# Kernel optimization log

Measured on AMD Instinct MI355X. Metric: run time of the kernel, lower is better.

Reference implementation:

```python
import jax, jax.numpy as jnp
import numpy as np

NUM_HEADS = 8  # matches init_kwargs


def setup_inputs() -> dict:
    key = jax.random.key(0)
    k_x, k_q, k_k, k_v, k_o = jax.random.split(key, 5)
    C = 512
    scale = 1.0 / np.sqrt(C).astype(np.float32)
    return {
        "x": jax.random.normal(k_x, (4, C, 1024), dtype=jnp.float32),
        "Wq": jax.random.normal(k_q, (C, C), dtype=jnp.float32) * scale,
        "Wk": jax.random.normal(k_k, (C, C), dtype=jnp.float32) * scale,
        "Wv": jax.random.normal(k_v, (C, C), dtype=jnp.float32) * scale,
        "Wo": jax.random.normal(k_o, (C, C), dtype=jnp.float32) * scale,
    }


def reference(x, Wq, Wk, Wv, Wo):
    # x: (b, C, n). Conv1d with kernel size 1 and no bias == channel matmul.
    b, C, n = x.shape
    H = NUM_HEADS
    d = C // H  # truncated_planes

    # 1x1 conv projections: (o, c) x (b, c, n) -> (b, o, n)
    q = jnp.einsum("oc,bcn->bon", Wq, x).reshape(b * H, d, n)
    k = jnp.einsum("oc,bcn->bon", Wk, x).reshape(b * H, d, n)
    v = jnp.einsum("oc,bcn->bon", Wv, x).reshape(b * H, d, n)

    # SelfAttention, embedded-gaussian mode (non-local block style, no 1/sqrt(d) scale):
    # scores[bh, i, j] = q[:, i] . k[:, j]; softmax over j; y = attn @ v
    scores = jnp.einsum("hdi,hdj->hij", q, k)       # (b*H, n, n)
    attn = jax.nn.softmax(scores, axis=-1)
    y = jnp.einsum("hij,hdj->hdi", attn, v)          # (b*H, d, n)

    y = y.reshape(b, C, n)
    out = jnp.einsum("oc,bcn->bon", Wo, y)           # final 1x1 conv
    return out
```

## Files before the change

### kernel.cpp

```cpp
#include <hip/hip_runtime.h>

typedef __attribute__((ext_vector_type(8))) short short8;
typedef __attribute__((ext_vector_type(8))) _Float16 half8;
typedef __attribute__((ext_vector_type(4))) float floatx4;
typedef __attribute__((ext_vector_type(4))) float floatv4;
typedef __attribute__((ext_vector_type(4))) short short4v;
typedef __attribute__((ext_vector_type(4))) unsigned short ushort4v;
typedef unsigned short u16;

#define MFMA_BF16(a,b,c) __builtin_amdgcn_mfma_f32_16x16x32_bf16((a),(b),(c),0,0,0)
#define MFMA_F16(a,b,c)  __builtin_amdgcn_mfma_f32_16x16x32_f16((a),(b),(c),0,0,0)

__device__ __forceinline__ u16 f2bf(float f) {
    union { float f; unsigned u; } v; v.f = f;
    unsigned r = (v.u + 0x7fffu + ((v.u >> 16) & 1u)) >> 16;
    return (u16)r;
}
__device__ __forceinline__ float bf2f(u16 h) {
    union { unsigned u; float f; } v; v.u = ((unsigned)h) << 16;
    return v.f;
}
__device__ __forceinline__ u16 f2h(float f) {
    union { _Float16 h; u16 u; } v; v.h = (_Float16)f;
    return v.u;
}

__device__ __forceinline__ void gll16(const u16* g, u16* l) {
    __builtin_amdgcn_global_load_lds(
        (const __attribute__((address_space(1))) void*)g,
        (__attribute__((address_space(3))) void*)l, 16, 0, 0);
}

__global__ __launch_bounds__(256) void prep_kernel(
    const void* __restrict__ x,
    const void* __restrict__ Wq, const void* __restrict__ Wk,
    const void* __restrict__ Wv, const void* __restrict__ Wo,
    u16* __restrict__ xT,
    u16* __restrict__ Wqh, u16* __restrict__ Wkh,
    u16* __restrict__ Wvh, u16* __restrict__ Woh,
    int* __restrict__ flag)
{
    __shared__ float tile[64][65];
    __shared__ int sflag;
    const int tid = threadIdx.x;

    if (tid < 64) {
        u16 u = ((const u16*)x)[2 * tid];
        int e = (u >> 7) & 0xFF;
        unsigned long long m = __ballot(e >= 96 && e <= 140);
        if (tid == 0) sflag = (__popcll(m) >= 40) ? 0 : 1;
    }
    __syncthreads();
    const int isf32 = sflag;
    const int bid = blockIdx.x;
    if (bid == 0 && tid == 0) *flag = isf32;

    if (bid < 512) {
        const int b = bid >> 7, rem = bid & 127;
        const int c0 = (rem >> 4) * 64, n0 = (rem & 15) * 64;
        const int cr = tid >> 4;
        const int n4 = (tid & 15) * 4;
        const size_t base = (size_t)b * 512 * 1024;
        #pragma unroll
        for (int i = 0; i < 4; ++i) {
            int c = i * 16 + cr;
            size_t idx = base + (size_t)(c0 + c) * 1024 + n0 + n4;
            float v0, v1, v2, v3;
            if (isf32) {
                floatv4 v = *(const floatv4*)((const float*)x + idx);
                v0 = v[0]; v1 = v[1]; v2 = v[2]; v3 = v[3];
            } else {
                ushort4v u = *(const ushort4v*)((const u16*)x + idx);
                v0 = bf2f(u[0]); v1 = bf2f(u[1]); v2 = bf2f(u[2]); v3 = bf2f(u[3]);
            }
            tile[c][n4 + 0] = v0; tile[c][n4 + 1] = v1;
            tile[c][n4 + 2] = v2; tile[c][n4 + 3] = v3;
        }
        __syncthreads();
        const int nr = tid >> 4;
        const int c4 = (tid & 15) * 4;
        #pragma unroll
        for (int i = 0; i < 4; ++i) {
            int n = i * 16 + nr;
            short4v o;
            o[0] = (short)f2h(tile[c4 + 0][n]);
            o[1] = (short)f2h(tile[c4 + 1][n]);
            o[2] = (short)f2h(tile[c4 + 2][n]);
            o[3] = (short)f2h(tile[c4 + 3][n]);
            *(short4v*)(xT + ((size_t)b * 1024 + n0 + n) * 512 + c0 + c4) = o;
        }
    } else {
        const int b2 = bid - 512;
        #pragma unroll
        for (int m = 0; m < 4; ++m) {
            const void* src = (m == 0) ? Wq : (m == 1) ? Wk : (m == 2) ? Wv : Wo;
            u16* dst = (m == 0) ? Wqh : (m == 1) ? Wkh : (m == 2) ? Wvh : Woh;
            #pragma unroll
            for (int j = 0; j < 4; ++j) {
                int i = b2 * 4096 + j * 1024 + tid * 4;
                short4v o;
                if (isf32) {
                    floatv4 v = *(const floatv4*)((const float*)src + i);
                    o[0] = (short)f2h(v[0]); o[1] = (short)f2h(v[1]);
                    o[2] = (short)f2h(v[2]); o[3] = (short)f2h(v[3]);
                } else {
                    ushort4v u = *(const ushort4v*)((const u16*)src + i);
                    o[0] = (short)f2h(bf2f(u[0])); o[1] = (short)f2h(bf2f(u[1]));
                    o[2] = (short)f2h(bf2f(u[2])); o[3] = (short)f2h(bf2f(u[3]));
                }
                *(short4v*)(dst + i) = o;
            }
        }
    }
}

__device__ __forceinline__ void stage_1t(
    const u16* __restrict__ A, const u16* __restrict__ B,
    u16* L, int k0, int wave, int srow, int koff)
{
    #pragma unroll
    for (int i = 0; i < 3; ++i) {
        int idx = wave + i * 4;
        const u16* s;
        if (idx < 4) s = A + (idx * 16 + srow) * 512 + k0 + koff;
        else         s = B + ((idx - 4) * 16 + srow) * 512 + k0 + koff;
        gll16(s, L + idx * 512);
    }
}

__device__ __forceinline__ void gemm_1t(
    const u16* __restrict__ A, const u16* __restrict__ B,
    u16* lds, floatx4 acc[2][4], int lane, int wave)
{
    const int quad = lane >> 4, l16 = lane & 15;
    const int msub = (wave & 1) * 32, nsub = (wave >> 1) * 64;
    const int srow = lane >> 2;
    const int koff = (((lane & 3) - (srow >> 1)) & 3) * 8;
    const int pA = ((quad + (l16 >> 1)) & 3) * 8;

    stage_1t(A, B, lds, 0, wave, srow, koff);
    for (int k0 = 0; k0 < 512; k0 += 32) {
        __syncthreads();
        u16* L = lds + ((k0 >> 5) & 1) * 6144;
        if (k0 + 32 < 512)
            stage_1t(A, B, lds + (((k0 >> 5) + 1) & 1) * 6144,
                     k0 + 32, wave, srow, koff);

        half8 ah[2], bh[4];
        #pragma unroll
        for (int mt = 0; mt < 2; ++mt)
            ah[mt] = *(const half8*)(L + (msub + mt * 16 + l16) * 32 + pA);
        #pragma unroll
        for (int nt = 0; nt < 4; ++nt)
            bh[nt] = *(const half8*)(L + 2048 + (nsub + nt * 16 + l16) * 32 + pA);
        #pragma unroll
        for (int mt = 0; mt < 2; ++mt)
            #pragma unroll
            for (int nt = 0; nt < 4; ++nt)
                acc[mt][nt] = MFMA_F16(ah[mt], bh[nt], acc[mt][nt]);
    }
}

__global__ __launch_bounds__(256) void proj_kernel(
    const u16* __restrict__ xT,
    const u16* __restrict__ Wqh, const u16* __restrict__ Wkh,
    const u16* __restrict__ Wvh,
    u16* __restrict__ qT, u16* __restrict__ kT,
    u16* __restrict__ vbuf)
{
    __shared__ u16 lds[12288];
    const int lane = threadIdx.x & 63;
    const int wave = threadIdx.x >> 6;
    const int quad = lane >> 4, l16 = lane & 15;
    const int idx = blockIdx.x;
    const int msub = (wave & 1) * 32, nsub = (wave >> 1) * 64;

    floatx4 acc[2][4];
    #pragma unroll
    for (int i = 0; i < 2; ++i)
        #pragma unroll
        for (int j = 0; j < 4; ++j) acc[i][j] = (floatx4){0.f, 0.f, 0.f, 0.f};

    if (idx < 512) {
        const int w = idx >> 8;
        const int rem = idx & 255;
        const int m0 = (rem >> 2) * 64;
        const int oblk = (rem & 3) * 128;
        gemm_1t(xT + (size_t)m0 * 512, ((w == 0) ? Wqh : Wkh) + oblk * 512,
                lds, acc, lane, wave);

        u16* dst = (w == 0) ? qT : kT;
        #pragma unroll
        for (int mt = 0; mt < 2; ++mt)
            #pragma unroll
            for (int r = 0; r < 4; ++r) {
                int row = m0 + msub + mt * 16 + quad * 4 + r;
                int b = row >> 10, n = row & 1023;
                #pragma unroll
                for (int nt = 0; nt < 4; ++nt) {
                    int o = oblk + nsub + nt * 16 + l16;
                    int head = b * 8 + (o >> 6);
                    int dd = o & 63;
                    dst[(head * 1024 + n) * 64 + dd] = f2h(acc[mt][nt][r]);
                }
            }
    } else {
        const int rem = idx - 512;
        const int m0 = (rem >> 5) * 64;
        const int nblk = (rem & 31) * 128;
        gemm_1t(Wvh + m0 * 512, xT + (size_t)nblk * 512, lds, acc, lane, wave);

        #pragma unroll
        for (int mt = 0; mt < 2; ++mt)
            #pragma unroll
            for (int r = 0; r < 4; ++r) {
                int o = m0 + msub + mt * 16 + quad * 4 + r;
                #pragma unroll
                for (int nt = 0; nt < 4; ++nt) {
                    int col = nblk + nsub + nt * 16 + l16;
                    int b = col >> 10, n = col & 1023;
                    vbuf[b * 524288 + o * 1024 + n] = f2bf(acc[mt][nt][r]);
                }
            }
    }
}

__global__ __launch_bounds__(512) void attn_kernel(
    const u16* __restrict__ qT, const u16* __restrict__ kT,
    const u16* __restrict__ vbuf,
    u16* __restrict__ yT)
{
    __shared__ u16 lds[16384];
    const int lane = threadIdx.x & 63;
    const int wave = threadIdx.x >> 6;
    const int quad = lane >> 4, l16 = lane & 15;
    const int head = blockIdx.x;
    const int i0 = blockIdx.y * 128 + wave * 16;
    const int b = head >> 3, h = head & 7;
    const u16* qp = qT + head * 65536;
    const u16* kp = kT + head * 65536;
    const u16* vb = vbuf + b * 524288 + h * 65536;
    const int srow = lane >> 2;
    const int koff = (((lane & 3) - (srow >> 1)) & 3) * 8;
    const int pA = ((quad + (l16 >> 1)) & 3) * 8;

    const int qoff = (i0 + l16) * 64 + quad * 8;
    half8 aq0 = *(const half8*)(qp + qoff);
    half8 aq1 = *(const half8*)(qp + qoff + 32);

    float lsum = 0.f;
    floatx4 oacc[4];
    #pragma unroll
    for (int dt = 0; dt < 4; ++dt) oacc[dt] = (floatx4){0.f, 0.f, 0.f, 0.f};

    const float L2E = 1.44269504f;
    const float C2  = 69.2493619f;

    auto stage_kv = [&](int j0, u16* L) {
        #pragma unroll
        for (int i = 0; i < 2; ++i) {
            int c = wave + i * 8;
            const u16* s;
            if (c < 8) {
                int kc = c >> 2, r0 = (c & 3) * 16;
                s = kp + (j0 + r0 + srow) * 64 + kc * 32 + koff;
            } else {
                int c8 = c - 8, js = c8 >> 2, r0 = (c8 & 3) * 16;
                s = vb + (r0 + srow) * 1024 + j0 + js * 32 + koff;
            }
            gll16(s, L + c * 512);
        }
    };

    stage_kv(0, lds);

    const int srcA = (quad & 1) * 32 + l16;
    const int srcB = srcA + 16;
    const bool hi = (quad >> 1) != 0;

    for (int j0 = 0; j0 < 1024; j0 += 64) {
        __syncthreads();
        u16* L = lds + ((j0 >> 6) & 1) * 8192;
        if (j0 + 64 < 1024)
            stage_kv(j0 + 64, lds + (((j0 >> 6) + 1) & 1) * 8192);

        unsigned pk[4][2];
        #pragma unroll
        for (int jt = 0; jt < 4; ++jt) {
            int off = jt * 512 + l16 * 32 + pA;
            half8 kh0 = *(const half8*)(L + off);
            half8 kh1 = *(const half8*)(L + 2048 + off);
            floatx4 s = {0.f, 0.f, 0.f, 0.f};
            s = MFMA_F16(kh0, aq0, s);
            s = MFMA_F16(kh1, aq1, s);
            float p0 = __builtin_amdgcn_exp2f(s[0] * L2E - C2);
            float p1 = __builtin_amdgcn_exp2f(s[1] * L2E - C2);
            float p2 = __builtin_amdgcn_exp2f(s[2] * L2E - C2);
            float p3 = __builtin_amdgcn_exp2f(s[3] * L2E - C2);
            lsum += (p0 + p1) + (p2 + p3);
            pk[jt][0] = (unsigned)f2bf(p0) | ((unsigned)f2bf(p1) << 16);
            pk[jt][1] = (unsigned)f2bf(p2) | ((unsigned)f2bf(p3) << 16);
        }

        #pragma unroll
        for (int jc = 0; jc < 2; ++jc) {
            unsigned a0 = (unsigned)__shfl((int)pk[jc * 2][0], srcA);
            unsigned b0 = (unsigned)__shfl((int)pk[jc * 2 + 1][0], srcA);
            unsigned a1 = (unsigned)__shfl((int)pk[jc * 2][1], srcA);
            unsigned b1 = (unsigned)__shfl((int)pk[jc * 2 + 1][1], srcA);
            unsigned a2 = (unsigned)__shfl((int)pk[jc * 2][0], srcB);
            unsigned b2 = (unsigned)__shfl((int)pk[jc * 2 + 1][0], srcB);
            unsigned a3 = (unsigned)__shfl((int)pk[jc * 2][1], srcB);
            unsigned b3 = (unsigned)__shfl((int)pk[jc * 2 + 1][1], srcB);
            union { unsigned u[4]; short8 s8; } pu;
            pu.u[0] = hi ? b0 : a0;
            pu.u[1] = hi ? b1 : a1;
            pu.u[2] = hi ? b2 : a2;
            pu.u[3] = hi ? b3 : a3;
            short8 pfrag = pu.s8;
            #pragma unroll
            for (int dt = 0; dt < 4; ++dt) {
                int off = dt * 512 + l16 * 32 + pA;
                short8 vv = *(const short8*)(L + 4096 + jc * 2048 + off);
                oacc[dt] = MFMA_BF16(vv, pfrag, oacc[dt]);
            }
        }
    }

    lsum += __shfl_xor(lsum, 16);
    lsum += __shfl_xor(lsum, 32);
    const float linv = 1.0f / lsum;

    u16* yrow = yT + ((size_t)b * 1024 + i0 + l16) * 512 + h * 64;
    #pragma unroll
    for (int dt = 0; dt < 4; ++dt) {
        short4v o;
        #pragma unroll
        for (int r = 0; r < 4; ++r) o[r] = (short)f2h(oacc[dt][r] * linv);
        *(short4v*)(yrow + dt * 16 + quad * 4) = o;
    }
}

__global__ __launch_bounds__(256) void out_kernel(
    const u16* __restrict__ Woh, const u16* __restrict__ yT,
    void* __restrict__ out, const int* __restrict__ flag)
{
    __shared__ u16 lds[12288];
    const int isf32 = *flag;
    const int lane = threadIdx.x & 63;
    const int wave = threadIdx.x >> 6;
    const int quad = lane >> 4, l16 = lane & 15;
    const int nblk = blockIdx.x * 128;
    const int oblk = blockIdx.y * 64;

    floatx4 acc[2][4];
    #pragma unroll
    for (int i = 0; i < 2; ++i)
        #pragma unroll
        for (int j = 0; j < 4; ++j) acc[i][j] = (floatx4){0.f, 0.f, 0.f, 0.f};

    gemm_1t(Woh + oblk * 512, yT + (size_t)nblk * 512, lds, acc, lane, wave);

    const int msub = (wave & 1) * 32, nsub = (wave >> 1) * 64;
    #pragma unroll
    for (int mt = 0; mt < 2; ++mt)
        #pragma unroll
        for (int r = 0; r < 4; ++r) {
            int o = oblk + msub + mt * 16 + quad * 4 + r;
            #pragma unroll
            for (int nt = 0; nt < 4; ++nt) {
                int col = nblk + nsub + nt * 16 + l16;
                int b = col >> 10, n = col & 1023;
                size_t di = (size_t)b * 524288 + o * 1024 + n;
                if (isf32) ((float*)out)[di] = acc[mt][nt][r];
                else       ((u16*)out)[di] = f2bf(acc[mt][nt][r]);
            }
        }
}

extern "C" void kernel_launch(void* const* d_in, const int* in_sizes, int n_in,
                              void* d_out, int out_size, void* d_ws, size_t ws_size,
                              hipStream_t stream)
{
    const void* x  = d_in[0];
    const void* Wq = d_in[1];
    const void* Wk = d_in[2];
    const void* Wv = d_in[3];
    const void* Wo = d_in[4];

    const int NX = 4 * 512 * 1024;
    const int NW = 512 * 512;

    char* p = (char*)d_ws;
    int* flag = (int*)p; p += 64;
    u16* xT   = (u16*)p; p += (size_t)NX * 2;
    u16* Wqh  = (u16*)p; p += (size_t)NW * 2;
    u16* Wkh  = (u16*)p; p += (size_t)NW * 2;
    u16* Wvh  = (u16*)p; p += (size_t)NW * 2;
    u16* Woh  = (u16*)p; p += (size_t)NW * 2;
    u16* qT   = (u16*)p; p += (size_t)NX * 2;
    u16* kT   = (u16*)p; p += (size_t)NX * 2;
    u16* vbuf = (u16*)p; p += (size_t)NX * 2;
    u16* ybuf = (u16*)p; p += (size_t)NX * 2;

    prep_kernel<<<576, 256, 0, stream>>>(
        x, Wq, Wk, Wv, Wo, xT, Wqh, Wkh, Wvh, Woh, flag);
    proj_kernel<<<768, 256, 0, stream>>>(
        xT, Wqh, Wkh, Wvh, qT, kT, vbuf);
    attn_kernel<<<dim3(32, 8), 512, 0, stream>>>(
        qT, kT, vbuf, ybuf);
    out_kernel<<<dim3(32, 8), 256, 0, stream>>>(
        Woh, ybuf, d_out, flag);
}
```

Baseline: 117.7 us.

## Use 128x128 GEMM tiles and one fused QKV projection over concatenated weights

Stores Wq, Wk and Wv contiguously so the projection becomes a single (4096 x 512) by (512 x 1536) GEMM. Both projection and output GEMMs move from 64x128 to 128x128 block tiles with 4x4 MFMA tiles per wave. The V projection is now computed in the same orientation as Q and K and written transposed into vbuf. Larger tiles raise operand reuse and cut global and LDS traffic per FLOP, at the cost of more registers, more LDS, and fewer blocks (384 and 128), which may underfill the GPU's compute units.

```diff
diff --git a/kernel.cpp b/kernel.cpp
--- a/kernel.cpp
+++ b/kernel.cpp
@@ -35,9 +35,7 @@
     const void* __restrict__ x,
     const void* __restrict__ Wq, const void* __restrict__ Wk,
     const void* __restrict__ Wv, const void* __restrict__ Wo,
-    u16* __restrict__ xT,
-    u16* __restrict__ Wqh, u16* __restrict__ Wkh,
-    u16* __restrict__ Wvh, u16* __restrict__ Woh,
+    u16* __restrict__ xT, u16* __restrict__ Wall, u16* __restrict__ Wo16,
     int* __restrict__ flag)
 {
     __shared__ float tile[64][65];
@@ -94,7 +92,7 @@
         #pragma unroll
         for (int m = 0; m < 4; ++m) {
             const void* src = (m == 0) ? Wq : (m == 1) ? Wk : (m == 2) ? Wv : Wo;
-            u16* dst = (m == 0) ? Wqh : (m == 1) ? Wkh : (m == 2) ? Wvh : Woh;
+            u16* dst = (m == 3) ? Wo16 : (Wall + m * 262144);
             #pragma unroll
             for (int j = 0; j < 4; ++j) {
                 int i = b2 * 4096 + j * 1024 + tid * 4;
@@ -114,47 +112,47 @@
     }
 }
 
-__device__ __forceinline__ void stage_1t(
+__device__ __forceinline__ void stage_2t(
     const u16* __restrict__ A, const u16* __restrict__ B,
     u16* L, int k0, int wave, int srow, int koff)
 {
     #pragma unroll
-    for (int i = 0; i < 3; ++i) {
+    for (int i = 0; i < 4; ++i) {
         int idx = wave + i * 4;
         const u16* s;
-        if (idx < 4) s = A + (idx * 16 + srow) * 512 + k0 + koff;
-        else         s = B + ((idx - 4) * 16 + srow) * 512 + k0 + koff;
+        if (idx < 8) s = A + (idx * 16 + srow) * 512 + k0 + koff;
+        else         s = B + ((idx - 8) * 16 + srow) * 512 + k0 + koff;
         gll16(s, L + idx * 512);
     }
 }
 
-__device__ __forceinline__ void gemm_1t(
+__device__ __forceinline__ void gemm_2t(
     const u16* __restrict__ A, const u16* __restrict__ B,
-    u16* lds, floatx4 acc[2][4], int lane, int wave)
+    u16* lds, floatx4 acc[4][4], int lane, int wave)
 {
     const int quad = lane >> 4, l16 = lane & 15;
-    const int msub = (wave & 1) * 32, nsub = (wave >> 1) * 64;
+    const int msub = (wave & 1) * 64, nsub = (wave >> 1) * 64;
     const int srow = lane >> 2;
     const int koff = (((lane & 3) - (srow >> 1)) & 3) * 8;
     const int pA = ((quad + (l16 >> 1)) & 3) * 8;
 
-    stage_1t(A, B, lds, 0, wave, srow, koff);
+    stage_2t(A, B, lds, 0, wave, srow, koff);
     for (int k0 = 0; k0 < 512; k0 += 32) {
         __syncthreads();
-        u16* L = lds + ((k0 >> 5) & 1) * 6144;
+        u16* L = lds + ((k0 >> 5) & 1) * 8192;
         if (k0 + 32 < 512)
-            stage_1t(A, B, lds + (((k0 >> 5) + 1) & 1) * 6144,
+            stage_2t(A, B, lds + (((k0 >> 5) + 1) & 1) * 8192,
                      k0 + 32, wave, srow, koff);
 
-        half8 ah[2], bh[4];
-        #pragma unroll
-        for (int mt = 0; mt < 2; ++mt)
+        half8 ah[4], bh[4];
+        #pragma unroll
+        for (int mt = 0; mt < 4; ++mt)
             ah[mt] = *(const half8*)(L + (msub + mt * 16 + l16) * 32 + pA);
         #pragma unroll
         for (int nt = 0; nt < 4; ++nt)
-            bh[nt] = *(const half8*)(L + 2048 + (nsub + nt * 16 + l16) * 32 + pA);
-        #pragma unroll
-        for (int mt = 0; mt < 2; ++mt)
+            bh[nt] = *(const half8*)(L + 4096 + (nsub + nt * 16 + l16) * 32 + pA);
+        #pragma unroll
+        for (int mt = 0; mt < 4; ++mt)
             #pragma unroll
             for (int nt = 0; nt < 4; ++nt)
                 acc[mt][nt] = MFMA_F16(ah[mt], bh[nt], acc[mt][nt]);
@@ -162,63 +160,54 @@
 }
 
 __global__ __launch_bounds__(256) void proj_kernel(
-    const u16* __restrict__ xT,
-    const u16* __restrict__ Wqh, const u16* __restrict__ Wkh,
-    const u16* __restrict__ Wvh,
+    const u16* __restrict__ xT, const u16* __restrict__ Wall,
     u16* __restrict__ qT, u16* __restrict__ kT,
     u16* __restrict__ vbuf)
 {
-    __shared__ u16 lds[12288];
+    __shared__ u16 lds[16384];
     const int lane = threadIdx.x & 63;
     const int wave = threadIdx.x >> 6;
     const int quad = lane >> 4, l16 = lane & 15;
-    const int idx = blockIdx.x;
-    const int msub = (wave & 1) * 32, nsub = (wave >> 1) * 64;
-
-    floatx4 acc[2][4];
-    #pragma unroll
-    for (int i = 0; i < 2; ++i)
+    const int m0 = blockIdx.x * 128;
+    const int oblk = blockIdx.y * 128;
+    const int msub = (wave & 1) * 64, nsub = (wave >> 1) * 64;
+
+    floatx4 acc[4][4];
+    #pragma unroll
+    for (int i = 0; i < 4; ++i)
         #pragma unroll
         for (int j = 0; j < 4; ++j) acc[i][j] = (floatx4){0.f, 0.f, 0.f, 0.f};
 
-    if (idx < 512) {
-        const int w = idx >> 8;
-        const int rem = idx & 255;
-        const int m0 = (rem >> 2) * 64;
-        const int oblk = (rem & 3) * 128;
-        gemm_1t(xT + (size_t)m0 * 512, ((w == 0) ? Wqh : Wkh) + oblk * 512,
-                lds, acc, lane, wave);
-
-        u16* dst = (w == 0) ? qT : kT;
-        #pragma unroll
-        for (int mt = 0; mt < 2; ++mt)
+    gemm_2t(xT + (size_t)m0 * 512, Wall + (size_t)oblk * 512, lds, acc, lane, wave);
+
+    if (oblk < 1024) {
+        u16* dst = (oblk < 512) ? qT : kT;
+        const int obase = oblk & 511;
+        #pragma unroll
+        for (int mt = 0; mt < 4; ++mt)
             #pragma unroll
             for (int r = 0; r < 4; ++r) {
                 int row = m0 + msub + mt * 16 + quad * 4 + r;
                 int b = row >> 10, n = row & 1023;
                 #pragma unroll
                 for (int nt = 0; nt < 4; ++nt) {
-                    int o = oblk + nsub + nt * 16 + l16;
+                    int o = obase + nsub + nt * 16 + l16;
                     int head = b * 8 + (o >> 6);
                     int dd = o & 63;
                     dst[(head * 1024 + n) * 64 + dd] = f2h(acc[mt][nt][r]);
                 }
             }
     } else {
-        const int rem = idx - 512;
-        const int m0 = (rem >> 5) * 64;
-        const int nblk = (rem & 31) * 128;
-        gemm_1t(Wvh + m0 * 512, xT + (size_t)nblk * 512, lds, acc, lane, wave);
-
-        #pragma unroll
-        for (int mt = 0; mt < 2; ++mt)
+        const int obase = oblk - 1024;
+        #pragma unroll
+        for (int mt = 0; mt < 4; ++mt)
             #pragma unroll
             for (int r = 0; r < 4; ++r) {
-                int o = m0 + msub + mt * 16 + quad * 4 + r;
+                int row = m0 + msub + mt * 16 + quad * 4 + r;
+                int b = row >> 10, n = row & 1023;
                 #pragma unroll
                 for (int nt = 0; nt < 4; ++nt) {
-                    int col = nblk + nsub + nt * 16 + l16;
-                    int b = col >> 10, n = col & 1023;
+                    int o = obase + nsub + nt * 16 + l16;
                     vbuf[b * 524288 + o * 1024 + n] = f2bf(acc[mt][nt][r]);
                 }
             }
@@ -345,25 +334,25 @@
     const u16* __restrict__ Woh, const u16* __restrict__ yT,
     void* __restrict__ out, const int* __restrict__ flag)
 {
-    __shared__ u16 lds[12288];
+    __shared__ u16 lds[16384];
     const int isf32 = *flag;
     const int lane = threadIdx.x & 63;
     const int wave = threadIdx.x >> 6;
     const int quad = lane >> 4, l16 = lane & 15;
     const int nblk = blockIdx.x * 128;
-    const int oblk = blockIdx.y * 64;
-
-    floatx4 acc[2][4];
-    #pragma unroll
-    for (int i = 0; i < 2; ++i)
+    const int oblk = blockIdx.y * 128;
+
+    floatx4 acc[4][4];
+    #pragma unroll
+    for (int i = 0; i < 4; ++i)
         #pragma unroll
         for (int j = 0; j < 4; ++j) acc[i][j] = (floatx4){0.f, 0.f, 0.f, 0.f};
 
-    gemm_1t(Woh + oblk * 512, yT + (size_t)nblk * 512, lds, acc, lane, wave);
-
-    const int msub = (wave & 1) * 32, nsub = (wave >> 1) * 64;
-    #pragma unroll
-    for (int mt = 0; mt < 2; ++mt)
+    gemm_2t(Woh + (size_t)oblk * 512, yT + (size_t)nblk * 512, lds, acc, lane, wave);
+
+    const int msub = (wave & 1) * 64, nsub = (wave >> 1) * 64;
+    #pragma unroll
+    for (int mt = 0; mt < 4; ++mt)
         #pragma unroll
         for (int r = 0; r < 4; ++r) {
             int o = oblk + msub + mt * 16 + quad * 4 + r;
@@ -394,9 +383,7 @@
     char* p = (char*)d_ws;
     int* flag = (int*)p; p += 64;
     u16* xT   = (u16*)p; p += (size_t)NX * 2;
-    u16* Wqh  = (u16*)p; p += (size_t)NW * 2;
-    u16* Wkh  = (u16*)p; p += (size_t)NW * 2;
-    u16* Wvh  = (u16*)p; p += (size_t)NW * 2;
+    u16* Wall = (u16*)p; p += (size_t)NW * 3 * 2;
     u16* Woh  = (u16*)p; p += (size_t)NW * 2;
     u16* qT   = (u16*)p; p += (size_t)NX * 2;
     u16* kT   = (u16*)p; p += (size_t)NX * 2;
@@ -404,11 +391,11 @@
     u16* ybuf = (u16*)p; p += (size_t)NX * 2;
 
     prep_kernel<<<576, 256, 0, stream>>>(
-        x, Wq, Wk, Wv, Wo, xT, Wqh, Wkh, Wvh, Woh, flag);
-    proj_kernel<<<768, 256, 0, stream>>>(
-        xT, Wqh, Wkh, Wvh, qT, kT, vbuf);
+        x, Wq, Wk, Wv, Wo, xT, Wall, Woh, flag);
+    proj_kernel<<<dim3(32, 12), 256, 0, stream>>>(
+        xT, Wall, qT, kT, vbuf);
     attn_kernel<<<dim3(32, 8), 512, 0, stream>>>(
         qT, kT, vbuf, ybuf);
-    out_kernel<<<dim3(32, 8), 256, 0, stream>>>(
+    out_kernel<<<dim3(32, 4), 256, 0, stream>>>(
         Woh, ybuf, d_out, flag);
 }
```

New measurement: 120.0 us. Within noise of the previous version (+2.0%).

## Unify QKV projection as one weight-major GEMM and halve attention block size

Applied to the files above, without the earlier changes.

Concatenates Wq/Wk/Wv into one contiguous weight buffer so the projection kernel runs a single 2D grid of weight-row by token-column tiles, with Q/K outputs written as packed 4-element vector stores instead of scalar scattered stores. The attention kernel drops from 512 to 256 threads per block (64 query rows per block), doubling the grid to 512 blocks and having each wave stage more K/V chunks. This aims to improve store coalescing and CU occupancy/load balance, at the cost of more K/V reloading per query row.

```diff
diff --git a/kernel.cpp b/kernel.cpp
--- a/kernel.cpp
+++ b/kernel.cpp
@@ -35,9 +35,7 @@
     const void* __restrict__ x,
     const void* __restrict__ Wq, const void* __restrict__ Wk,
     const void* __restrict__ Wv, const void* __restrict__ Wo,
-    u16* __restrict__ xT,
-    u16* __restrict__ Wqh, u16* __restrict__ Wkh,
-    u16* __restrict__ Wvh, u16* __restrict__ Woh,
+    u16* __restrict__ xT, u16* __restrict__ Wall, u16* __restrict__ Wo16,
     int* __restrict__ flag)
 {
     __shared__ float tile[64][65];
@@ -94,7 +92,7 @@
         #pragma unroll
         for (int m = 0; m < 4; ++m) {
             const void* src = (m == 0) ? Wq : (m == 1) ? Wk : (m == 2) ? Wv : Wo;
-            u16* dst = (m == 0) ? Wqh : (m == 1) ? Wkh : (m == 2) ? Wvh : Woh;
+            u16* dst = (m == 3) ? Wo16 : (Wall + m * 262144);
             #pragma unroll
             for (int j = 0; j < 4; ++j) {
                 int i = b2 * 4096 + j * 1024 + tid * 4;
@@ -162,9 +160,7 @@
 }
 
 __global__ __launch_bounds__(256) void proj_kernel(
-    const u16* __restrict__ xT,
-    const u16* __restrict__ Wqh, const u16* __restrict__ Wkh,
-    const u16* __restrict__ Wvh,
+    const u16* __restrict__ xT, const u16* __restrict__ Wall,
     u16* __restrict__ qT, u16* __restrict__ kT,
     u16* __restrict__ vbuf)
 {
@@ -172,7 +168,8 @@
     const int lane = threadIdx.x & 63;
     const int wave = threadIdx.x >> 6;
     const int quad = lane >> 4, l16 = lane & 15;
-    const int idx = blockIdx.x;
+    const int m0 = blockIdx.x * 128;
+    const int oblk = blockIdx.y * 64;
     const int msub = (wave & 1) * 32, nsub = (wave >> 1) * 64;
 
     floatx4 acc[2][4];
@@ -181,43 +178,33 @@
         #pragma unroll
         for (int j = 0; j < 4; ++j) acc[i][j] = (floatx4){0.f, 0.f, 0.f, 0.f};
 
-    if (idx < 512) {
-        const int w = idx >> 8;
-        const int rem = idx & 255;
-        const int m0 = (rem >> 2) * 64;
-        const int oblk = (rem & 3) * 128;
-        gemm_1t(xT + (size_t)m0 * 512, ((w == 0) ? Wqh : Wkh) + oblk * 512,
-                lds, acc, lane, wave);
-
-        u16* dst = (w == 0) ? qT : kT;
+    gemm_1t(Wall + (size_t)oblk * 512, xT + (size_t)m0 * 512, lds, acc, lane, wave);
+
+    if (oblk < 1024) {
+        u16* dst = (oblk < 512) ? qT : kT;
+        #pragma unroll
+        for (int mt = 0; mt < 2; ++mt) {
+            int od = (oblk & 511) + msub + mt * 16 + quad * 4;
+            int hsub = od >> 6, dd0 = od & 63;
+            #pragma unroll
+            for (int nt = 0; nt < 4; ++nt) {
+                int col = m0 + nsub + nt * 16 + l16;
+                int b = col >> 10, n = col & 1023;
+                short4v o4;
+                #pragma unroll
+                for (int r = 0; r < 4; ++r) o4[r] = (short)f2h(acc[mt][nt][r]);
+                *(short4v*)(dst + ((size_t)(b * 8 + hsub) * 1024 + n) * 64 + dd0) = o4;
+            }
+        }
+    } else {
         #pragma unroll
         for (int mt = 0; mt < 2; ++mt)
             #pragma unroll
             for (int r = 0; r < 4; ++r) {
-                int row = m0 + msub + mt * 16 + quad * 4 + r;
-                int b = row >> 10, n = row & 1023;
+                int o = (oblk - 1024) + msub + mt * 16 + quad * 4 + r;
                 #pragma unroll
                 for (int nt = 0; nt < 4; ++nt) {
-                    int o = oblk + nsub + nt * 16 + l16;
-                    int head = b * 8 + (o >> 6);
-                    int dd = o & 63;
-                    dst[(head * 1024 + n) * 64 + dd] = f2h(acc[mt][nt][r]);
-                }
-            }
-    } else {
-        const int rem = idx - 512;
-        const int m0 = (rem >> 5) * 64;
-        const int nblk = (rem & 31) * 128;
-        gemm_1t(Wvh + m0 * 512, xT + (size_t)nblk * 512, lds, acc, lane, wave);
-
-        #pragma unroll
-        for (int mt = 0; mt < 2; ++mt)
-            #pragma unroll
-            for (int r = 0; r < 4; ++r) {
-                int o = m0 + msub + mt * 16 + quad * 4 + r;
-                #pragma unroll
-                for (int nt = 0; nt < 4; ++nt) {
-                    int col = nblk + nsub + nt * 16 + l16;
+                    int col = m0 + nsub + nt * 16 + l16;
                     int b = col >> 10, n = col & 1023;
                     vbuf[b * 524288 + o * 1024 + n] = f2bf(acc[mt][nt][r]);
                 }
@@ -225,7 +212,7 @@
     }
 }
 
-__global__ __launch_bounds__(512) void attn_kernel(
+__global__ __launch_bounds__(256) void attn_kernel(
     const u16* __restrict__ qT, const u16* __restrict__ kT,
     const u16* __restrict__ vbuf,
     u16* __restrict__ yT)
@@ -235,7 +222,7 @@
     const int wave = threadIdx.x >> 6;
     const int quad = lane >> 4, l16 = lane & 15;
     const int head = blockIdx.x;
-    const int i0 = blockIdx.y * 128 + wave * 16;
+    const int i0 = blockIdx.y * 64 + wave * 16;
     const int b = head >> 3, h = head & 7;
     const u16* qp = qT + head * 65536;
     const u16* kp = kT + head * 65536;
@@ -258,8 +245,8 @@
 
     auto stage_kv = [&](int j0, u16* L) {
         #pragma unroll
-        for (int i = 0; i < 2; ++i) {
-            int c = wave + i * 8;
+        for (int i = 0; i < 4; ++i) {
+            int c = wave + i * 4;
             const u16* s;
             if (c < 8) {
                 int kc = c >> 2, r0 = (c & 3) * 16;
@@ -359,7 +346,7 @@
         #pragma unroll
         for (int j = 0; j < 4; ++j) acc[i][j] = (floatx4){0.f, 0.f, 0.f, 0.f};
 
-    gemm_1t(Woh + oblk * 512, yT + (size_t)nblk * 512, lds, acc, lane, wave);
+    gemm_1t(Woh + (size_t)oblk * 512, yT + (size_t)nblk * 512, lds, acc, lane, wave);
 
     const int msub = (wave & 1) * 32, nsub = (wave >> 1) * 64;
     #pragma unroll
@@ -394,9 +381,7 @@
     char* p = (char*)d_ws;
     int* flag = (int*)p; p += 64;
     u16* xT   = (u16*)p; p += (size_t)NX * 2;
-    u16* Wqh  = (u16*)p; p += (size_t)NW * 2;
-    u16* Wkh  = (u16*)p; p += (size_t)NW * 2;
-    u16* Wvh  = (u16*)p; p += (size_t)NW * 2;
+    u16* Wall = (u16*)p; p += (size_t)NW * 3 * 2;
     u16* Woh  = (u16*)p; p += (size_t)NW * 2;
     u16* qT   = (u16*)p; p += (size_t)NX * 2;
     u16* kT   = (u16*)p; p += (size_t)NX * 2;
@@ -404,10 +389,10 @@
     u16* ybuf = (u16*)p; p += (size_t)NX * 2;
 
     prep_kernel<<<576, 256, 0, stream>>>(
-        x, Wq, Wk, Wv, Wo, xT, Wqh, Wkh, Wvh, Woh, flag);
-    proj_kernel<<<768, 256, 0, stream>>>(
-        xT, Wqh, Wkh, Wvh, qT, kT, vbuf);
-    attn_kernel<<<dim3(32, 8), 512, 0, stream>>>(
+        x, Wq, Wk, Wv, Wo, xT, Wall, Woh, flag);
+    proj_kernel<<<dim3(32, 24), 256, 0, stream>>>(
+        xT, Wall, qT, kT, vbuf);
+    attn_kernel<<<dim3(32, 16), 256, 0, stream>>>(
         qT, kT, vbuf, ybuf);
     out_kernel<<<dim3(32, 8), 256, 0, stream>>>(
         Woh, ybuf, d_out, flag);
```

Measured after the change: 117.7 us. No clear change (+0.0%).
